# Kernel optimization log

Hardware: AMD Instinct MI355X
Metric: run time of the kernel (lower is better)

## Reference

```python
import jax, jax.numpy as jnp
import numpy as np

B, S, D, H = 2, 2048, 1024, 16
DK = D // H


def setup_inputs() -> dict:
    key = jax.random.key(0)
    ks = jax.random.split(key, 12)
    s = 0.02
    return {
        "q": jax.random.normal(ks[0], (B, S, D), jnp.float32),
        "k": jax.random.normal(ks[1], (B, S, D), jnp.float32),
        "v": jax.random.normal(ks[2], (B, S, D), jnp.float32),
        "mask": jax.random.randint(ks[3], (1, 1, S, S), 0, 2, jnp.int32),
        "Wq": jax.random.normal(ks[4], (D, D), jnp.float32) * s,
        "bq": jnp.zeros((D,), jnp.float32),
        "Wk": jax.random.normal(ks[5], (D, D), jnp.float32) * s,
        "bk": jnp.zeros((D,), jnp.float32),
        "Wv": jax.random.normal(ks[6], (D, D), jnp.float32) * s,
        "bv": jnp.zeros((D,), jnp.float32),
        "Wo": jax.random.normal(ks[7], (D, D), jnp.float32) * s,
        "bo": jnp.zeros((D,), jnp.float32),
    }


def reference(q, k, v, mask, Wq, bq, Wk, bk, Wv, bv, Wo, bo):
    # linear projections (torch Linear: x @ W.T + b)
    qp = q @ Wq.T + bq
    kp = k @ Wk.T + bk
    vp = v @ Wv.T + bv
    # [B, S, D] -> [B, H, S, DK]
    split = lambda x: x.reshape(B, S, H, DK).transpose(0, 2, 1, 3)
    qh, kh, vh = split(qp), split(kp), split(vp)
    scale = 1.0 / jnp.sqrt(jnp.float32(DK))
    attn = jnp.einsum('bhsd,bhtd->bhst', qh, kh) * scale  # [B,H,S,S]
    attn = jnp.where(mask == 0, jnp.float32(-1e9), attn)
    attn = jax.nn.softmax(attn, axis=-1)
    out = jnp.einsum('bhst,bhtd->bhsd', attn, vh)  # [B,H,S,DK]
    concat = out.transpose(0, 2, 1, 3).reshape(B, S, D)
    return concat @ Wo.T + bo
```

## Files before the change

### kernel.cpp

```cpp
#include <hip/hip_runtime.h>
#include <hip/hip_bf16.h>


using bf16x8 = __attribute__((ext_vector_type(8))) short;
using f32x4  = __attribute__((ext_vector_type(4))) float;
using f32x16 = __attribute__((ext_vector_type(16))) float;

constexpr int Bc = 2, Sc = 2048, Dc = 1024, Hc = 16, DKc = 64;
constexpr int Mc = Bc * Sc;
#define QSCALE 0.18033688011112042f

__device__ __forceinline__ void lds_load16(const void* g, void* l) {
  __builtin_amdgcn_global_load_lds(
      (const __attribute__((address_space(1))) unsigned int*)g,
      (__attribute__((address_space(3))) unsigned int*)l, 16, 0, 0);
}

#if __has_builtin(__builtin_amdgcn_exp2f)
__device__ __forceinline__ float exp2_fast(float x) { return __builtin_amdgcn_exp2f(x); }
#else
__device__ __forceinline__ float exp2_fast(float x) {
  float r;
  asm("v_exp_f32 %0, %1\n\ts_nop 0" : "=v"(r) : "v"(x));
  return r;
}
#endif

__device__ __forceinline__ unsigned cvt_pk_bf16(float lo, float hi) {
  unsigned r;
  asm("v_cvt_pk_bf16_f32 %0, %1, %2" : "=v"(r) : "v"(lo), "v"(hi));
  return r;
}

#define PSWAP(A, B) \
  asm volatile("v_permlane32_swap_b32 %0, %1" : "+v"(A), "+v"(B))

__device__ __forceinline__ unsigned pack2bf(float a, float b) {
  union { __hip_bfloat16 h; unsigned short s; } ua, ub;
  ua.h = __float2bfloat16(a);
  ub.h = __float2bfloat16(b);
  return (unsigned)ua.s | ((unsigned)ub.s << 16);
}

__global__ void prep(const float* __restrict__ q, const float* __restrict__ k,
                     const float* __restrict__ v, const int* __restrict__ mask,
                     const float* __restrict__ Wq, const float* __restrict__ Wk,
                     const float* __restrict__ Wv, const float* __restrict__ Wo,
                     char* __restrict__ ws) {
  const size_t MB = 1024 * 1024;
  int blk = blockIdx.x;
  int tid = threadIdx.x;
  if (blk < 6144) {
    int which = blk >> 11;
    int i = (((blk & 2047) << 8) + tid) * 8;
    const float* s = which == 0 ? q : (which == 1 ? k : v);
    __hip_bfloat16* d = (__hip_bfloat16*)(ws + (size_t)which * 8 * MB);
    float4 x = *(const float4*)&s[i];
    float4 y = *(const float4*)&s[i + 4];
    uint4 pk = {pack2bf(x.x, x.y), pack2bf(x.z, x.w),
                pack2bf(y.x, y.y), pack2bf(y.z, y.w)};
    *(uint4*)&d[i] = pk;
  } else if (blk < 8192) {
    int bb = blk - 6144;
    int which = bb >> 9;
    int i = (((bb & 511) << 8) + tid) * 8;
    const float* s = which == 0 ? Wq : (which == 1 ? Wk : (which == 2 ? Wv : Wo));
    __hip_bfloat16* d = which < 3 ? (__hip_bfloat16*)(ws + (24 + 2 * which) * MB)
                                  : (__hip_bfloat16*)(ws + 30 * MB);
    float4 x = *(const float4*)&s[i];
    float4 y = *(const float4*)&s[i + 4];
    uint4 pk = {pack2bf(x.x, x.y), pack2bf(x.z, x.w),
                pack2bf(y.x, y.y), pack2bf(y.z, y.w)};
    *(uint4*)&d[i] = pk;
  } else {
    int blkm = blk - 8192;
    int i0 = ((blkm << 8) + tid) * 4;
    uint4 m = *(const uint4*)&mask[i0];
    unsigned nib = (m.x != 0 ? 1u : 0u) | (m.y != 0 ? 2u : 0u) |
                   (m.z != 0 ? 4u : 0u) | (m.w != 0 ? 8u : 0u);
    unsigned long long w = (unsigned long long)nib << (4 * (tid & 15));
    w |= __shfl_xor(w, 1);
    w |= __shfl_xor(w, 2);
    w |= __shfl_xor(w, 4);
    w |= __shfl_xor(w, 8);
    if ((tid & 15) == 0)
      ((unsigned long long*)(ws + 32 * MB))[(blkm << 4) + (tid >> 4)] = w;
  }
}

__global__ __launch_bounds__(256, 3) void proj_qkv(
    const __hip_bfloat16* __restrict__ qb, const __hip_bfloat16* __restrict__ kb,
    const __hip_bfloat16* __restrict__ vb, const __hip_bfloat16* __restrict__ Wcat,
    const float* __restrict__ bq, const float* __restrict__ bk,
    const float* __restrict__ bv, __hip_bfloat16* __restrict__ qhd,
    __hip_bfloat16* __restrict__ khd, __hip_bfloat16* __restrict__ vtd) {
  __shared__ __align__(16) __hip_bfloat16 As[2][128 * 32];
  __shared__ __align__(16) __hip_bfloat16 Bs[2][128 * 32];
  const int tid = threadIdx.x;
  const int f = blockIdx.x, g = f >> 3;
  const int m0 = ((f & 7) * 4 + g / 24) * 128;
  const int n0 = (g % 24) * 128;
  const int which = n0 >> 10, nl0 = n0 & 1023;
  const __hip_bfloat16* X = which == 0 ? qb : (which == 1 ? kb : vb);
  const float* bias = which == 0 ? bq : (which == 1 ? bk : bv);
  const int w = tid >> 6, lane = tid & 63, ln = lane & 15, quad = lane >> 4;
  const int rl = w * 32 + (lane >> 2);
  const int sw8 = ((lane & 3) ^ ((lane >> 2) & 3)) * 8;
  const int aoff = (n0 + rl) * 1024 + sw8;
  const int boff = (m0 + rl) * 1024 + sw8;
  char* aDst = (char*)As + w * 2048 + lane * 16;
  char* bDst = (char*)Bs + w * 2048 + lane * 16;
  const int rkq = (quad ^ (ln & 3)) * 16;
  const int rA0 = ((w >> 1) * 64 + ln) * 64 + rkq;
  const int rB0 = ((w & 1) * 64 + ln) * 64 + rkq;
  f32x4 acc[4][4] = {};

#define PSTAGE(KO, BI)                                                        \
  {                                                                           \
    lds_load16(&Wcat[aoff + (KO)], aDst + (BI)*8192);                         \
    lds_load16(&Wcat[aoff + 16384 + (KO)], aDst + (BI)*8192 + 1024);          \
    lds_load16(&X[boff + (KO)], bDst + (BI)*8192);                            \
    lds_load16(&X[boff + 16384 + (KO)], bDst + (BI)*8192 + 1024);             \
  }

  PSTAGE(0, 0);
  if (which == 2) {
    for (int kb32 = 0; kb32 < 32; ++kb32) {
      const int bi = kb32 & 1;
      __syncthreads();
      if (kb32 < 31) PSTAGE((kb32 + 1) * 32, bi ^ 1);
      bf16x8 af[4], bf[4];
#pragma unroll
      for (int i = 0; i < 4; ++i)
        af[i] = *(bf16x8*)((char*)As + bi * 8192 + rA0 + i * 1024);
#pragma unroll
      for (int j = 0; j < 4; ++j)
        bf[j] = *(bf16x8*)((char*)Bs + bi * 8192 + rB0 + j * 1024);
#pragma unroll
      for (int i = 0; i < 4; ++i)
#pragma unroll
        for (int j = 0; j < 4; ++j)
          acc[i][j] = __builtin_amdgcn_mfma_f32_16x16x32_bf16(bf[j], af[i],
                                                              acc[i][j], 0, 0, 0);
    }
  } else {
    for (int kb32 = 0; kb32 < 32; ++kb32) {
      const int bi = kb32 & 1;
      __syncthreads();
      if (kb32 < 31) PSTAGE((kb32 + 1) * 32, bi ^ 1);
      bf16x8 af[4], bf[4];
#pragma unroll
      for (int i = 0; i < 4; ++i)
        af[i] = *(bf16x8*)((char*)As + bi * 8192 + rA0 + i * 1024);
#pragma unroll
      for (int j = 0; j < 4; ++j)
        bf[j] = *(bf16x8*)((char*)Bs + bi * 8192 + rB0 + j * 1024);
#pragma unroll
      for (int i = 0; i < 4; ++i)
#pragma unroll
        for (int j = 0; j < 4; ++j)
          acc[i][j] = __builtin_amdgcn_mfma_f32_16x16x32_bf16(af[i], bf[j],
                                                              acc[i][j], 0, 0, 0);
    }
  }

  const int wA = (w >> 1) * 64, wB = (w & 1) * 64;
  if (which == 2) {
#pragma unroll
    for (int i = 0; i < 4; ++i) {
      int nf = nl0 + wA + i * 16 + ln;
      int h = nf >> 6, dk = nf & 63;
      float bb = bias[nf];
#pragma unroll
      for (int j = 0; j < 4; ++j) {
        int sb = m0 + wB + j * 16 + quad * 4;
        int b = sb >> 11, s = sb & 2047;
        float vv[4] = {acc[i][j][0] + bb, acc[i][j][1] + bb,
                       acc[i][j][2] + bb, acc[i][j][3] + bb};
        uint2 pk = {pack2bf(vv[0], vv[1]), pack2bf(vv[2], vv[3])};
        *(uint2*)&vtd[(((size_t)(b * Hc + h) * DKc + dk) * Sc) + s] = pk;
      }
    }
  } else {
#pragma unroll
    for (int i = 0; i < 4; ++i) {
      int nfb = nl0 + wA + i * 16 + quad * 4;
      float4 b4 = *(const float4*)&bias[nfb];
      int h = nfb >> 6, dk0 = nfb & 63;
#pragma unroll
      for (int j = 0; j < 4; ++j) {
        int sg = m0 + wB + j * 16 + ln;
        int b = sg >> 11, s = sg & 2047;
        float vv[4] = {acc[i][j][0] + b4.x, acc[i][j][1] + b4.y,
                       acc[i][j][2] + b4.z, acc[i][j][3] + b4.w};
        if (which == 0) {
          uint2 pk = {pack2bf(vv[0] * QSCALE, vv[1] * QSCALE),
                      pack2bf(vv[2] * QSCALE, vv[3] * QSCALE)};
          *(uint2*)&qhd[(((size_t)(b * Hc + h) * Sc + s) * DKc) + dk0] = pk;
        } else {
          uint2 pk = {pack2bf(vv[0], vv[1]), pack2bf(vv[2], vv[3])};
          *(uint2*)&khd[(((size_t)(b * Hc + h) * Sc + s) * DKc) + dk0] = pk;
        }
      }
    }
  }
}

__global__ __launch_bounds__(256, 2) void gemm_out(
    const __hip_bfloat16* __restrict__ X, const __hip_bfloat16* __restrict__ W,
    const float* __restrict__ bias, float* __restrict__ Y) {
  __shared__ __align__(16) __hip_bfloat16 As[2][64 * 64];
  __shared__ __align__(16) __hip_bfloat16 Bs[2][128 * 64];
  const int tid = threadIdx.x;
  const int f = blockIdx.x, g = f >> 3;
  const int m0 = ((f & 7) * 4 + (g >> 4)) * 128;
  const int n0 = (g & 15) * 64;
  const int w = tid >> 6, lane = tid & 63, ln = lane & 15, quad = lane >> 4;
  const int wA = (w & 1) * 32, wB = (w >> 1) * 64;
  const int swz = ((lane & 7) ^ (lane >> 3)) * 8;
  const int rk0 = ln * 128 + ((quad ^ (ln & 7)) * 16);
  const int rk1 = ln * 128 + (((quad + 4) ^ (ln & 7)) * 16);
  const int aoff = (n0 + w * 16 + (lane >> 3)) * 1024 + swz;
  const int boff = (m0 + w * 32 + (lane >> 3)) * 1024 + swz;
  f32x4 acc[2][4] = {};

#define OSTAGE(KO, BI)                                                        \
  {                                                                           \
    _Pragma("unroll") for (int i = 0; i < 2; ++i)                             \
        lds_load16(&W[aoff + i * 8192 + (KO)],                                \
                   (char*)As[BI] + w * 2048 + lane * 16 + i * 1024);          \
    _Pragma("unroll") for (int i = 0; i < 4; ++i)                             \
        lds_load16(&X[boff + i * 8192 + (KO)],                                \
                   (char*)Bs[BI] + w * 4096 + lane * 16 + i * 1024);          \
  }

  OSTAGE(0, 0);
  for (int kb64 = 0; kb64 < 16; ++kb64) {
    const int bi = kb64 & 1;
    __syncthreads();
    if (kb64 + 1 < 16) OSTAGE((kb64 + 1) * 64, bi ^ 1);
    bf16x8 af[2][2], bf[4][2];
#pragma unroll
    for (int i = 0; i < 2; ++i) {
      af[i][0] = *(bf16x8*)((char*)As[bi] + wA * 128 + i * 2048 + rk0);
      af[i][1] = *(bf16x8*)((char*)As[bi] + wA * 128 + i * 2048 + rk1);
    }
#pragma unroll
    for (int j = 0; j < 4; ++j) {
      bf[j][0] = *(bf16x8*)((char*)Bs[bi] + wB * 128 + j * 2048 + rk0);
      bf[j][1] = *(bf16x8*)((char*)Bs[bi] + wB * 128 + j * 2048 + rk1);
    }
#pragma unroll
    for (int i = 0; i < 2; ++i)
#pragma unroll
      for (int j = 0; j < 4; ++j) {
        acc[i][j] = __builtin_amdgcn_mfma_f32_16x16x32_bf16(af[i][0], bf[j][0],
                                                            acc[i][j], 0, 0, 0);
        acc[i][j] = __builtin_amdgcn_mfma_f32_16x16x32_bf16(af[i][1], bf[j][1],
                                                            acc[i][j], 0, 0, 0);
      }
  }
#pragma unroll
  for (int i = 0; i < 2; ++i) {
    int nfb = n0 + wA + i * 16 + quad * 4;
    float4 b4 = *(const float4*)&bias[nfb];
#pragma unroll
    for (int j = 0; j < 4; ++j) {
      int sg = m0 + wB + j * 16 + ln;
      float4 st = {acc[i][j][0] + b4.x, acc[i][j][1] + b4.y,
                   acc[i][j][2] + b4.z, acc[i][j][3] + b4.w};
      *(float4*)&Y[(size_t)sg * Dc + nfb] = st;
    }
  }
}

__global__ __launch_bounds__(256, 2) void flash_attn(
    const __hip_bfloat16* __restrict__ qh, const __hip_bfloat16* __restrict__ kh,
    const __hip_bfloat16* __restrict__ vt, const uint2* __restrict__ mb2,
    __hip_bfloat16* __restrict__ oc) {
  __shared__ __align__(16) char L[49152];
  const int tid = threadIdx.x;
  const int f = blockIdx.x, g = f >> 3;
  const int bh = (f & 7) * 4 + (g >> 4);
  const int q0 = (g & 15) * 128;
  const int b = bh >> 4, h = bh & 15;
  const int w = tid >> 6, lane = tid & 63, l31 = lane & 31, hi = lane >> 5;
  const size_t base = (size_t)bh * Sc * DKc;
  const __hip_bfloat16* khb = kh + base;
  const __hip_bfloat16* vtb = vt + base;
  const int qglob = q0 + w * 32 + l31;

  bf16x8 qf[4];
#pragma unroll
  for (int dt = 0; dt < 4; ++dt)
    qf[dt] = *(const bf16x8*)&qh[base + (size_t)qglob * 64 + dt * 16 + hi * 8];

  bf16x8 onesA;
#pragma unroll
  for (int i = 0; i < 8; ++i) onesA[i] = (short)0x3F80;

  const int trow = tid >> 3, tcol = tid & 7;
  const int kbase = trow * 64 + ((tcol ^ (trow & 7)) * 8);
  const int vbase = trow * 2048 + ((tcol ^ (trow & 7)) * 8);
  char* Ld = L + tid * 16;

  const int rowb = l31 * 128;
  const int xs = lane & 7;

  f32x16 Oacc0 = {}, Oacc1 = {}, lacc = {};
  bf16x8 pbC[4];
  f32x16 cA, cB;

#define STAGE_OFF(BOFF, T)                                                    \
  {                                                                           \
    lds_load16(khb + kbase + (T)*4096,        Ld + (BOFF));                   \
    lds_load16(khb + kbase + (T)*4096 + 2048, Ld + (BOFF) + 4096);            \
    lds_load16(vtb + vbase + (T)*64,          Ld + 24576 + (BOFF));           \
    lds_load16(vtb + vbase + (T)*64 + 65536,  Ld + 24576 + (BOFF) + 4096);    \
  }

#define QKT_SUB(BOFF, SUB, CV)                                                \
  {                                                                           \
    bf16x8 kf0 = *(bf16x8*)(L + (BOFF) + (SUB)*4096 + rowb + (((0 + hi) ^ xs) * 16)); \
    bf16x8 kf1 = *(bf16x8*)(L + (BOFF) + (SUB)*4096 + rowb + (((2 + hi) ^ xs) * 16)); \
    bf16x8 kf2 = *(bf16x8*)(L + (BOFF) + (SUB)*4096 + rowb + (((4 + hi) ^ xs) * 16)); \
    bf16x8 kf3 = *(bf16x8*)(L + (BOFF) + (SUB)*4096 + rowb + (((6 + hi) ^ xs) * 16)); \
    f32x16 zz_ = {};                                                          \
    CV = __builtin_amdgcn_mfma_f32_32x32x16_bf16(kf0, qf[0], zz_, 0, 0, 0);   \
    CV = __builtin_amdgcn_mfma_f32_32x32x16_bf16(kf1, qf[1], CV, 0, 0, 0);    \
    CV = __builtin_amdgcn_mfma_f32_32x32x16_bf16(kf2, qf[2], CV, 0, 0, 0);    \
    CV = __builtin_amdgcn_mfma_f32_32x32x16_bf16(kf3, qf[3], CV, 0, 0, 0);    \
  }

#define SM_SUB(CV, MW, PB0, PB1)                                              \
  {                                                                           \
    unsigned shm = (MW) >> (hi * 4);                                          \
    float p[16];                                                              \
    _Pragma("unroll") for (int r = 0; r < 16; ++r) {                          \
      unsigned tg = shm >> (8 * (r >> 2));                                    \
      float e = exp2_fast(CV[r]);                                             \
      p[r] = (tg & (1u << (r & 3))) ? e : 0.f;                                \
    }                                                                         \
    unsigned w0 = cvt_pk_bf16(p[0], p[1]),   w1 = cvt_pk_bf16(p[2], p[3]);    \
    unsigned w2 = cvt_pk_bf16(p[4], p[5]),   w3 = cvt_pk_bf16(p[6], p[7]);    \
    unsigned w4 = cvt_pk_bf16(p[8], p[9]),   w5 = cvt_pk_bf16(p[10], p[11]);  \
    unsigned w6 = cvt_pk_bf16(p[12], p[13]), w7 = cvt_pk_bf16(p[14], p[15]);  \
    PSWAP(w0, w2); PSWAP(w1, w3); PSWAP(w4, w6); PSWAP(w5, w7);               \
    { union { unsigned u[4]; bf16x8 v; } tt_;                                 \
      tt_.u[0] = w0; tt_.u[1] = w1; tt_.u[2] = w2; tt_.u[3] = w3;             \
      PB0 = tt_.v; }                                                          \
    { union { unsigned u[4]; bf16x8 v; } tt_;                                 \
      tt_.u[0] = w4; tt_.u[1] = w5; tt_.u[2] = w6; tt_.u[3] = w7;             \
      PB1 = tt_.v; }                                                          \
  }

#define PV_CLUSTER(VOFF)                                                      \
  {                                                                           \
    __builtin_amdgcn_s_setprio(1);                                            \
    _Pragma("unroll") for (int kt = 0; kt < 4; ++kt) {                        \
      bf16x8 vf0 = *(bf16x8*)(L + 24576 + (VOFF) + rowb + (((kt * 2 + hi) ^ xs) * 16)); \
      bf16x8 vf1 = *(bf16x8*)(L + 24576 + (VOFF) + 4096 + rowb + (((kt * 2 + hi) ^ xs) * 16)); \
      lacc  = __builtin_amdgcn_mfma_f32_32x32x16_bf16(onesA, pbC[kt], lacc, 0, 0, 0); \
      Oacc0 = __builtin_amdgcn_mfma_f32_32x32x16_bf16(vf0, pbC[kt], Oacc0, 0, 0, 0);  \
      Oacc1 = __builtin_amdgcn_mfma_f32_32x32x16_bf16(vf1, pbC[kt], Oacc1, 0, 0, 0);  \
    }                                                                         \
    __builtin_amdgcn_s_setprio(0);                                            \
  }

  const uint2* mrow = mb2 + (size_t)qglob * 32;
  uint2 mbC = mrow[0];
  STAGE_OFF(0, 0);
  __syncthreads();
  uint2 mbN = mrow[1];
  STAGE_OFF(8192, 1);
  __builtin_amdgcn_s_setprio(1);
  QKT_SUB(0, 0, cA);
  QKT_SUB(0, 1, cB);
  __builtin_amdgcn_s_setprio(0);
  SM_SUB(cA, mbC.x, pbC[0], pbC[1]);
  SM_SUB(cB, mbC.y, pbC[2], pbC[3]);
  mbC = mbN;

  int curo = 8192, prevo = 0;
  for (int t = 1; t < 32; ++t) {
    __syncthreads();
    if (t < 31) {
      mbN = mrow[t + 1];
      int nxto = curo + 8192; if (nxto == 24576) nxto = 0;
      STAGE_OFF(nxto, t + 1);
    }
    __builtin_amdgcn_s_setprio(1);
    QKT_SUB(curo, 0, cA);
    QKT_SUB(curo, 1, cB);
    __builtin_amdgcn_s_setprio(0);
    PV_CLUSTER(prevo);
    SM_SUB(cA, mbC.x, pbC[0], pbC[1]);
    SM_SUB(cB, mbC.y, pbC[2], pbC[3]);
    prevo = curo;
    curo += 8192; if (curo == 24576) curo = 0;
    mbC = mbN;
  }
  PV_CLUSTER(prevo);

  float linv = 1.f / fmaxf(lacc[0], 1e-30f);
  const size_t obase = (size_t)(b * Sc + qglob) * Dc + h * 64;
#pragma unroll
  for (int gq = 0; gq < 4; ++gq) {
    int d0 = gq * 8 + hi * 4;
    uint2 pk0 = {pack2bf(Oacc0[4 * gq] * linv, Oacc0[4 * gq + 1] * linv),
                 pack2bf(Oacc0[4 * gq + 2] * linv, Oacc0[4 * gq + 3] * linv)};
    *(uint2*)&oc[obase + d0] = pk0;
    uint2 pk1 = {pack2bf(Oacc1[4 * gq] * linv, Oacc1[4 * gq + 1] * linv),
                 pack2bf(Oacc1[4 * gq + 2] * linv, Oacc1[4 * gq + 3] * linv)};
    *(uint2*)&oc[obase + 32 + d0] = pk1;
  }
#undef STAGE_OFF
#undef QKT_SUB
#undef SM_SUB
#undef PV_CLUSTER
}

extern "C" void kernel_launch(void* const* d_in, const int* in_sizes, int n_in,
                              void* d_out, int out_size, void* d_ws, size_t ws_size,
                              hipStream_t stream) {
  const float* q  = (const float*)d_in[0];
  const float* k  = (const float*)d_in[1];
  const float* v  = (const float*)d_in[2];
  const int* mask = (const int*)d_in[3];
  const float* Wq = (const float*)d_in[4];
  const float* bq = (const float*)d_in[5];
  const float* Wk = (const float*)d_in[6];
  const float* bk = (const float*)d_in[7];
  const float* Wv = (const float*)d_in[8];
  const float* bv = (const float*)d_in[9];
  const float* Wo = (const float*)d_in[10];
  const float* bo = (const float*)d_in[11];

  char* ws = (char*)d_ws;
  const size_t MB = 1024 * 1024;
  __hip_bfloat16* qb   = (__hip_bfloat16*)(ws + 0 * MB);
  __hip_bfloat16* kb   = (__hip_bfloat16*)(ws + 8 * MB);
  __hip_bfloat16* vb   = (__hip_bfloat16*)(ws + 16 * MB);
  __hip_bfloat16* Wcat = (__hip_bfloat16*)(ws + 24 * MB);
  __hip_bfloat16* Wob  = (__hip_bfloat16*)(ws + 30 * MB);
  uint2*          mb2  = (uint2*)(ws + 32 * MB);
  __hip_bfloat16* qhd  = (__hip_bfloat16*)(ws + 33 * MB);
  __hip_bfloat16* khd  = (__hip_bfloat16*)(ws + 41 * MB);
  __hip_bfloat16* vtd  = (__hip_bfloat16*)(ws + 49 * MB);
  __hip_bfloat16* oc   = (__hip_bfloat16*)(ws + 57 * MB);

  prep<<<12288, 256, 0, stream>>>(q, k, v, mask, Wq, Wk, Wv, Wo, ws);
  proj_qkv<<<768, 256, 0, stream>>>(qb, kb, vb, Wcat, bq, bk, bv, qhd, khd, vtd);
  flash_attn<<<512, 256, 0, stream>>>(qhd, khd, vtd, mb2, oc);
  gemm_out<<<512, 256, 0, stream>>>(oc, Wob, bo, (float*)d_out);
}
```

Baseline: 238.8 us.

## Fuse fp32-to-bf16 activation conversion into QKV projection GEMM

Result: slower. 255.0 us (+6.8%).

```diff
diff --git a/kernel.cpp b/kernel.cpp
--- a/kernel.cpp
+++ b/kernel.cpp
@@ -42,38 +42,25 @@
   return (unsigned)ua.s | ((unsigned)ub.s << 16);
 }
 
-__global__ void prep(const float* __restrict__ q, const float* __restrict__ k,
-                     const float* __restrict__ v, const int* __restrict__ mask,
+__global__ void prep(const int* __restrict__ mask,
                      const float* __restrict__ Wq, const float* __restrict__ Wk,
                      const float* __restrict__ Wv, const float* __restrict__ Wo,
                      char* __restrict__ ws) {
   const size_t MB = 1024 * 1024;
   int blk = blockIdx.x;
   int tid = threadIdx.x;
-  if (blk < 6144) {
-    int which = blk >> 11;
-    int i = (((blk & 2047) << 8) + tid) * 8;
-    const float* s = which == 0 ? q : (which == 1 ? k : v);
-    __hip_bfloat16* d = (__hip_bfloat16*)(ws + (size_t)which * 8 * MB);
-    float4 x = *(const float4*)&s[i];
-    float4 y = *(const float4*)&s[i + 4];
-    uint4 pk = {pack2bf(x.x, x.y), pack2bf(x.z, x.w),
-                pack2bf(y.x, y.y), pack2bf(y.z, y.w)};
-    *(uint4*)&d[i] = pk;
-  } else if (blk < 8192) {
-    int bb = blk - 6144;
-    int which = bb >> 9;
-    int i = (((bb & 511) << 8) + tid) * 8;
+  if (blk < 2048) {
+    int which = blk >> 9;
+    int i = (((blk & 511) << 8) + tid) * 8;
     const float* s = which == 0 ? Wq : (which == 1 ? Wk : (which == 2 ? Wv : Wo));
-    __hip_bfloat16* d = which < 3 ? (__hip_bfloat16*)(ws + (24 + 2 * which) * MB)
-                                  : (__hip_bfloat16*)(ws + 30 * MB);
+    __hip_bfloat16* d = (__hip_bfloat16*)(ws + (size_t)2 * which * MB);
     float4 x = *(const float4*)&s[i];
     float4 y = *(const float4*)&s[i + 4];
     uint4 pk = {pack2bf(x.x, x.y), pack2bf(x.z, x.w),
                 pack2bf(y.x, y.y), pack2bf(y.z, y.w)};
     *(uint4*)&d[i] = pk;
   } else {
-    int blkm = blk - 8192;
+    int blkm = blk - 2048;
     int i0 = ((blkm << 8) + tid) * 4;
     uint4 m = *(const uint4*)&mask[i0];
     unsigned nib = (m.x != 0 ? 1u : 0u) | (m.y != 0 ? 2u : 0u) |
@@ -84,43 +71,64 @@
     w |= __shfl_xor(w, 4);
     w |= __shfl_xor(w, 8);
     if ((tid & 15) == 0)
-      ((unsigned long long*)(ws + 32 * MB))[(blkm << 4) + (tid >> 4)] = w;
+      ((unsigned long long*)(ws + 8 * MB))[(blkm << 4) + (tid >> 4)] = w;
   }
 }
 
 __global__ __launch_bounds__(256, 3) void proj_qkv(
-    const __hip_bfloat16* __restrict__ qb, const __hip_bfloat16* __restrict__ kb,
-    const __hip_bfloat16* __restrict__ vb, const __hip_bfloat16* __restrict__ Wcat,
+    const float* __restrict__ qf_, const float* __restrict__ kf_,
+    const float* __restrict__ vf_, const __hip_bfloat16* __restrict__ Wcat,
     const float* __restrict__ bq, const float* __restrict__ bk,
     const float* __restrict__ bv, __hip_bfloat16* __restrict__ qhd,
     __hip_bfloat16* __restrict__ khd, __hip_bfloat16* __restrict__ vtd) {
   __shared__ __align__(16) __hip_bfloat16 As[2][128 * 32];
-  __shared__ __align__(16) __hip_bfloat16 Bs[2][128 * 32];
+  __shared__ __align__(16) float Bs[2][128 * 32];
   const int tid = threadIdx.x;
   const int f = blockIdx.x, g = f >> 3;
   const int m0 = ((f & 7) * 4 + g / 24) * 128;
   const int n0 = (g % 24) * 128;
   const int which = n0 >> 10, nl0 = n0 & 1023;
-  const __hip_bfloat16* X = which == 0 ? qb : (which == 1 ? kb : vb);
+  const float* X = which == 0 ? qf_ : (which == 1 ? kf_ : vf_);
   const float* bias = which == 0 ? bq : (which == 1 ? bk : bv);
   const int w = tid >> 6, lane = tid & 63, ln = lane & 15, quad = lane >> 4;
   const int rl = w * 32 + (lane >> 2);
   const int sw8 = ((lane & 3) ^ ((lane >> 2) & 3)) * 8;
   const int aoff = (n0 + rl) * 1024 + sw8;
-  const int boff = (m0 + rl) * 1024 + sw8;
   char* aDst = (char*)As + w * 2048 + lane * 16;
-  char* bDst = (char*)Bs + w * 2048 + lane * 16;
+  const int brow = tid >> 3;
+  const int bsw = ((tid & 7) ^ (brow & 7)) * 4;
+  const int xoff = (m0 + brow) * 1024 + bsw;
+  char* bDst = (char*)Bs + tid * 16;
   const int rkq = (quad ^ (ln & 3)) * 16;
   const int rA0 = ((w >> 1) * 64 + ln) * 64 + rkq;
-  const int rB0 = ((w & 1) * 64 + ln) * 64 + rkq;
+  const int rBbase = (((w & 1) * 64) + ln) * 128;
+  const int rBc0 = ((2 * quad + 0) ^ (ln & 7)) * 16;
+  const int rBc1 = ((2 * quad + 1) ^ (ln & 7)) * 16;
   f32x4 acc[4][4] = {};
 
 #define PSTAGE(KO, BI)                                                        \
   {                                                                           \
     lds_load16(&Wcat[aoff + (KO)], aDst + (BI)*8192);                         \
     lds_load16(&Wcat[aoff + 16384 + (KO)], aDst + (BI)*8192 + 1024);          \
-    lds_load16(&X[boff + (KO)], bDst + (BI)*8192);                            \
-    lds_load16(&X[boff + 16384 + (KO)], bDst + (BI)*8192 + 1024);             \
+    lds_load16(&X[xoff + 0 * 32768 + (KO)], bDst + (BI)*16384 + 0 * 4096);    \
+    lds_load16(&X[xoff + 1 * 32768 + (KO)], bDst + (BI)*16384 + 1 * 4096);    \
+    lds_load16(&X[xoff + 2 * 32768 + (KO)], bDst + (BI)*16384 + 2 * 4096);    \
+    lds_load16(&X[xoff + 3 * 32768 + (KO)], bDst + (BI)*16384 + 3 * 4096);    \
+  }
+
+#define LOAD_BF(BI)                                                           \
+  bf16x8 af[4], bf[4];                                                        \
+  _Pragma("unroll") for (int i = 0; i < 4; ++i)                               \
+      af[i] = *(bf16x8*)((char*)As + (BI)*8192 + rA0 + i * 1024);             \
+  _Pragma("unroll") for (int j = 0; j < 4; ++j) {                             \
+    f32x4 b0 = *(f32x4*)((char*)Bs + (BI)*16384 + rBbase + j * 2048 + rBc0);  \
+    f32x4 b1 = *(f32x4*)((char*)Bs + (BI)*16384 + rBbase + j * 2048 + rBc1);  \
+    union { unsigned u[4]; bf16x8 v; } tb;                                    \
+    tb.u[0] = cvt_pk_bf16(b0[0], b0[1]);                                      \
+    tb.u[1] = cvt_pk_bf16(b0[2], b0[3]);                                      \
+    tb.u[2] = cvt_pk_bf16(b1[0], b1[1]);                                      \
+    tb.u[3] = cvt_pk_bf16(b1[2], b1[3]);                                      \
+    bf[j] = tb.v;                                                             \
   }
 
   PSTAGE(0, 0);
@@ -129,13 +137,7 @@
       const int bi = kb32 & 1;
       __syncthreads();
       if (kb32 < 31) PSTAGE((kb32 + 1) * 32, bi ^ 1);
-      bf16x8 af[4], bf[4];
-#pragma unroll
-      for (int i = 0; i < 4; ++i)
-        af[i] = *(bf16x8*)((char*)As + bi * 8192 + rA0 + i * 1024);
-#pragma unroll
-      for (int j = 0; j < 4; ++j)
-        bf[j] = *(bf16x8*)((char*)Bs + bi * 8192 + rB0 + j * 1024);
+      LOAD_BF(bi);
 #pragma unroll
       for (int i = 0; i < 4; ++i)
 #pragma unroll
@@ -148,13 +150,7 @@
       const int bi = kb32 & 1;
       __syncthreads();
       if (kb32 < 31) PSTAGE((kb32 + 1) * 32, bi ^ 1);
-      bf16x8 af[4], bf[4];
-#pragma unroll
-      for (int i = 0; i < 4; ++i)
-        af[i] = *(bf16x8*)((char*)As + bi * 8192 + rA0 + i * 1024);
-#pragma unroll
-      for (int j = 0; j < 4; ++j)
-        bf[j] = *(bf16x8*)((char*)Bs + bi * 8192 + rB0 + j * 1024);
+      LOAD_BF(bi);
 #pragma unroll
       for (int i = 0; i < 4; ++i)
 #pragma unroll
@@ -204,6 +200,8 @@
       }
     }
   }
+#undef PSTAGE
+#undef LOAD_BF
 }
 
 __global__ __launch_bounds__(256, 2) void gemm_out(
@@ -438,19 +436,16 @@
 
   char* ws = (char*)d_ws;
   const size_t MB = 1024 * 1024;
-  __hip_bfloat16* qb   = (__hip_bfloat16*)(ws + 0 * MB);
-  __hip_bfloat16* kb   = (__hip_bfloat16*)(ws + 8 * MB);
-  __hip_bfloat16* vb   = (__hip_bfloat16*)(ws + 16 * MB);
-  __hip_bfloat16* Wcat = (__hip_bfloat16*)(ws + 24 * MB);
-  __hip_bfloat16* Wob  = (__hip_bfloat16*)(ws + 30 * MB);
-  uint2*          mb2  = (uint2*)(ws + 32 * MB);
-  __hip_bfloat16* qhd  = (__hip_bfloat16*)(ws + 33 * MB);
-  __hip_bfloat16* khd  = (__hip_bfloat16*)(ws + 41 * MB);
-  __hip_bfloat16* vtd  = (__hip_bfloat16*)(ws + 49 * MB);
-  __hip_bfloat16* oc   = (__hip_bfloat16*)(ws + 57 * MB);
-
-  prep<<<12288, 256, 0, stream>>>(q, k, v, mask, Wq, Wk, Wv, Wo, ws);
-  proj_qkv<<<768, 256, 0, stream>>>(qb, kb, vb, Wcat, bq, bk, bv, qhd, khd, vtd);
+  __hip_bfloat16* Wcat = (__hip_bfloat16*)(ws + 0 * MB);
+  __hip_bfloat16* Wob  = (__hip_bfloat16*)(ws + 6 * MB);
+  uint2*          mb2  = (uint2*)(ws + 8 * MB);
+  __hip_bfloat16* qhd  = (__hip_bfloat16*)(ws + 9 * MB);
+  __hip_bfloat16* khd  = (__hip_bfloat16*)(ws + 17 * MB);
+  __hip_bfloat16* vtd  = (__hip_bfloat16*)(ws + 25 * MB);
+  __hip_bfloat16* oc   = (__hip_bfloat16*)(ws + 33 * MB);
+
+  prep<<<6144, 256, 0, stream>>>(mask, Wq, Wk, Wv, Wo, ws);
+  proj_qkv<<<768, 256, 0, stream>>>(q, k, v, Wcat, bq, bk, bv, qhd, khd, vtd);
   flash_attn<<<512, 256, 0, stream>>>(qhd, khd, vtd, mb2, oc);
   gemm_out<<<512, 256, 0, stream>>>(oc, Wob, bo, (float*)d_out);
 }
```
